# Optimization experiments

Measured on AMD Instinct MI355X. Metric: run time of the kernel, lower is better.

## Reference

```python
import jax, jax.numpy as jnp
import numpy as np

B, N, D, H, F = 2, 2048, 512, 8, 2048
HD = D // H
EPS = 1e-5

def _ln(x, g, b):
    m = jnp.mean(x, axis=-1, keepdims=True)
    v = jnp.mean((x - m) ** 2, axis=-1, keepdims=True)
    return (x - m) * jax.lax.rsqrt(v + EPS) * g + b

def setup_inputs() -> dict:
    key = jax.random.key(0)
    ks = jax.random.split(key, 20)
    def lin(k, din, dout, std=0.05):
        kw, kb = jax.random.split(k)
        return (jax.random.normal(kw, (din, dout), jnp.float32) * std,
                jnp.zeros((dout,), jnp.float32))
    Wq, bq = lin(ks[0], D, D)
    Wk, bk = lin(ks[1], D, D)
    Wv, bv = lin(ks[2], D, D)
    Wg, bg = lin(ks[3], D, D)
    Wo, bo = lin(ks[4], D, D)
    W1, b1 = lin(ks[5], D, F)
    W2, b2 = lin(ks[6], F, D)
    return {
        'x': jax.random.normal(ks[7], (B, N, D), jnp.float32),
        'attn_bias': jax.random.normal(ks[8], (B, N, N, H), jnp.float32) * 0.1,
        'attn_mask': jnp.zeros((B, N, N), jnp.bool_),
        'Wq': Wq, 'bq': bq, 'Wk': Wk, 'bk': bk, 'Wv': Wv, 'bv': bv,
        'Wg': Wg, 'bg': bg, 'Wo': Wo, 'bo': bo,
        'ln1_g': jnp.ones((D,), jnp.float32), 'ln1_b': jnp.zeros((D,), jnp.float32),
        'ln2_g': jnp.ones((D,), jnp.float32), 'ln2_b': jnp.zeros((D,), jnp.float32),
        'W1': W1, 'b1': b1, 'W2': W2, 'b2': b2,
    }

def reference(x, attn_bias, attn_mask, Wq, bq, Wk, bk, Wv, bv, Wg, bg, Wo, bo,
              ln1_g, ln1_b, ln2_g, ln2_b, W1, b1, W2, b2):
    scaling = HD ** -0.5
    # --- self-attention sublayer (pre-LN) ---
    y = _ln(x, ln1_g, ln1_b)
    q = (y @ Wq + bq).reshape(B, N, H, HD) * scaling
    k = (y @ Wk + bk).reshape(B, N, H, HD)
    v = (y @ Wv + bv).reshape(B, N, H, HD)
    u = y * jax.nn.sigmoid(y @ Wg + bg)            # GLU gating branch
    scores = jnp.einsum('bqhd,bkhd->bqkh', q, k)   # [B, Nq, Nk, H]
    scores = scores + attn_bias                    # attn_bias_type == 'add'
    scores = jnp.where(attn_mask[..., None], -jnp.inf, scores)
    w = jax.nn.softmax(scores, axis=2)             # softmax over keys
    attn = jnp.einsum('bqkh,bkhd->bqhd', w, v).reshape(B, N, D)
    attn = attn @ Wo + bo
    y = u + attn
    x = x + y                                      # residual (dropout = identity, eval)
    # --- FFN sublayer (pre-LN) ---
    y = _ln(x, ln2_g, ln2_b)
    y = jax.nn.gelu(y @ W1 + b1, approximate=False) @ W2 + b2
    return x + y
```

## Files before the change

### kernel.cpp

```cpp
#include <hip/hip_runtime.h>
#include <hip/hip_bf16.h>

#define DI __device__ __forceinline__

typedef __attribute__((ext_vector_type(8))) __bf16 bf16x8;
typedef __attribute__((ext_vector_type(4))) float f32x4;
typedef __attribute__((ext_vector_type(4))) unsigned short u16x4;
typedef __attribute__((ext_vector_type(8))) unsigned short u16x8;

DI unsigned short f2bs(float f) {
  __hip_bfloat16 h = __float2bfloat16(f);
  return __builtin_bit_cast(unsigned short, h);
}
DI float bs2f(unsigned short s) {
  return __bfloat162float(__builtin_bit_cast(__hip_bfloat16, s));
}
DI f32x4 mfma16(bf16x8 a, bf16x8 b, f32x4 c) {
  return __builtin_amdgcn_mfma_f32_16x16x32_bf16(a, b, c, 0, 0, 0);
}
DI void g2lds16(const void* g, void* l) {
  __builtin_amdgcn_global_load_lds(
      (__attribute__((address_space(1))) void*)(unsigned long long)g,
      (__attribute__((address_space(3))) void*)l, 16, 0, 0);
}
DI void block_sync_lds() {
  asm volatile("s_waitcnt lgkmcnt(0)" ::: "memory");
  __builtin_amdgcn_sched_barrier(0);
  __builtin_amdgcn_s_barrier();
  __builtin_amdgcn_sched_barrier(0);
}

__global__ __launch_bounds__(256) void k_transw(const float* __restrict__ W,
                                                unsigned short* __restrict__ Wt,
                                                int K, int N) {
  __shared__ float tile[64][65];
  int tk = blockIdx.x * 64, tn = blockIdx.y * 64;
  int t = threadIdx.x;
#pragma unroll
  for (int i = 0; i < 16; ++i) {
    int idx = t + i * 256;
    int r = idx >> 6, c = idx & 63;
    tile[r][c] = W[(size_t)(tk + r) * N + tn + c];
  }
  __syncthreads();
#pragma unroll
  for (int i = 0; i < 16; ++i) {
    int idx = t + i * 256;
    int n = idx >> 6, kk = idx & 63;
    Wt[(size_t)(tn + n) * K + tk + kk] = f2bs(tile[kk][n]);
  }
}

__global__ __launch_bounds__(256) void k_bcat(const float* __restrict__ bq,
                                              const float* __restrict__ bk,
                                              const float* __restrict__ bv,
                                              const float* __restrict__ bg,
                                              float* __restrict__ bcat) {
  int t = blockIdx.x * 256 + threadIdx.x;
  const float* src = t < 512 ? bq : t < 1024 ? bk : t < 1536 ? bv : bg;
  bcat[t] = src[t & 511];
}

__global__ __launch_bounds__(256) void k_ln(const float* __restrict__ x,
                                            const float* __restrict__ g,
                                            const float* __restrict__ b,
                                            unsigned short* __restrict__ y) {
  int row = blockIdx.x, t = threadIdx.x;
  const float* xr = x + (size_t)row * 512;
  float a0 = xr[t], a1 = xr[t + 256];
  float s1 = a0 + a1, s2 = a0 * a0 + a1 * a1;
#pragma unroll
  for (int o = 32; o > 0; o >>= 1) {
    s1 += __shfl_down(s1, o);
    s2 += __shfl_down(s2, o);
  }
  __shared__ float r1[4], r2[4], bc[2];
  int w = t >> 6, l = t & 63;
  if (l == 0) { r1[w] = s1; r2[w] = s2; }
  __syncthreads();
  if (t == 0) {
    float t1 = r1[0] + r1[1] + r1[2] + r1[3];
    float t2 = r2[0] + r2[1] + r2[2] + r2[3];
    float m = t1 / 512.f;
    float v = t2 / 512.f - m * m;
    bc[0] = m;
    bc[1] = rsqrtf(v + 1e-5f);
  }
  __syncthreads();
  float m = bc[0], inv = bc[1];
  y[(size_t)row * 512 + t] = f2bs((a0 - m) * inv * g[t] + b[t]);
  y[(size_t)row * 512 + t + 256] = f2bs((a1 - m) * inv * g[t + 256] + b[t + 256]);
}

template <int BM>
__global__ __launch_bounds__(256) void k_gemm(
    const unsigned short* __restrict__ A, const unsigned short* __restrict__ Bt,
    const float* __restrict__ bias, int M, int N, int K, int mode,
    float* __restrict__ outf, unsigned short* __restrict__ outh,
    const float* __restrict__ add1, const float* __restrict__ add2,
    unsigned short* __restrict__ vtout) {
  constexpr int MI = BM / 32;
  __shared__ __align__(16) unsigned short lA[BM * 64];
  __shared__ __align__(16) unsigned short lB[64 * 64];
  int t = threadIdx.x, w = t >> 6, l = t & 63;
  int l15 = l & 15, lg = l >> 4;
  int m0 = blockIdx.x * BM, n0 = blockIdx.y * 64;
  int wm = (w >> 1) * (BM / 2), wn = (w & 1) * 32;
  f32x4 acc[MI][2] = {};
  int sr = l >> 3, scb = (l & 7) * 16;
  for (int k0 = 0; k0 < K; k0 += 64) {
#pragma unroll
    for (int c = 0; c < MI; ++c) {
      int row = w * (BM / 4) + sr + c * 8;
      g2lds16((const char*)A + ((size_t)(m0 + row) * K + k0) * 2 + scb,
              (char*)lA + w * (BM / 4) * 128 + c * 1024);
    }
#pragma unroll
    for (int c = 0; c < 2; ++c) {
      int row = w * 16 + sr + c * 8;
      g2lds16((const char*)Bt + ((size_t)(n0 + row) * K + k0) * 2 + scb,
              (char*)lB + w * 2048 + c * 1024);
    }
    __syncthreads();
#pragma unroll
    for (int kc = 0; kc < 2; ++kc) {
      bf16x8 af[MI], bfr[2];
#pragma unroll
      for (int i = 0; i < MI; ++i)
        af[i] = *(const bf16x8*)((const char*)lA + (wm + i * 16 + l15) * 128 + kc * 64 + lg * 16);
#pragma unroll
      for (int j = 0; j < 2; ++j)
        bfr[j] = *(const bf16x8*)((const char*)lB + (wn + j * 16 + l15) * 128 + kc * 64 + lg * 16);
#pragma unroll
      for (int i = 0; i < MI; ++i)
#pragma unroll
        for (int j = 0; j < 2; ++j)
          acc[i][j] = mfma16(af[i], bfr[j], acc[i][j]);
    }
    __syncthreads();
  }
#pragma unroll
  for (int i = 0; i < MI; ++i) {
#pragma unroll
    for (int j = 0; j < 2; ++j) {
      int col = n0 + wn + j * 16 + l15;
      int row0 = m0 + wm + i * 16 + lg * 4;
      float vals[4];
#pragma unroll
      for (int r = 0; r < 4; ++r) vals[r] = acc[i][j][r] + bias[col];
      if (mode == 6) {
        int sel = col >> 9, c5 = col & 511;
        if (sel == 2) {
          int hh = c5 >> 6, dd = c5 & 63, bb = row0 >> 11, nn = row0 & 2047;
          u16x4 pk;
#pragma unroll
          for (int r = 0; r < 4; ++r) pk[r] = f2bs(vals[r]);
          *(u16x4*)(vtout + (((size_t)(bb * 8 + hh) * 64 + dd) * 2048 + nn)) = pk;
        } else {
#pragma unroll
          for (int r = 0; r < 4; ++r) {
            size_t idx = (size_t)(row0 + r) * 512 + c5;
            if (sel == 0) outh[idx] = f2bs(vals[r] * 0.125f);
            else if (sel == 1) outh[2097152 + idx] = f2bs(vals[r]);
            else outf[idx] = bs2f(A[idx]) * (1.f / (1.f + __expf(-vals[r])));
          }
        }
      } else {
#pragma unroll
        for (int r = 0; r < 4; ++r) {
          size_t idx = (size_t)(row0 + r) * N + col;
          if (mode == 3) outf[idx] = vals[r] + add1[idx] + add2[idx];
          else if (mode == 4) outh[idx] = f2bs(0.5f * vals[r] * (1.f + erff(vals[r] * 0.70710678f)));
          else outf[idx] = vals[r] + add1[idx];
        }
      }
    }
  }
}

template <int NKS>
__global__ __launch_bounds__(512, 4) void k_attn11(
    const unsigned short* __restrict__ q, const unsigned short* __restrict__ kk,
    const unsigned short* __restrict__ vt, const float* __restrict__ bias,
    const unsigned char* __restrict__ mask, unsigned short* __restrict__ opart,
    float* __restrict__ lpart) {
  __shared__ __align__(16) unsigned short lsB[2][16 * 260];
  __shared__ __align__(16) unsigned short ls_p[8][16][36];

  int bid = blockIdx.x;
  int b = bid & 1;
  int rest = bid >> 1;
  int qt = rest & 127;
  int ksp = rest >> 7;
  int q0 = qt * 16;
  int kbase0 = ksp * (2048 / NKS);
  const int ITERS = 2048 / NKS / 32;
  int t = threadIdx.x, w = t >> 6, l = t & 63;
  int l15 = l & 15, lg = l >> 4;
  int h = w;

  bf16x8 qa0 = *(const bf16x8*)(q + ((size_t)(b * 2048 + q0 + l15) * 512 + h * 64 + lg * 8));
  bf16x8 qa1 = *(const bf16x8*)(q + ((size_t)(b * 2048 + q0 + l15) * 512 + h * 64 + 32 + lg * 8));

  union { bf16x8 v; unsigned short s[8]; } uo;
#pragma unroll
  for (int j = 0; j < 8; ++j) uo.s[j] = 0x3F80;
  const bf16x8 vones = uo.v;

  f32x4 oacc[4] = {};
  f32x4 lacc = {};

  const unsigned short* kbase = kk + ((size_t)(b * 2048) + l15) * 512 + h * 64 + lg * 8;
  const unsigned short* vbase = vt + ((size_t)(b * 8 + h) * 64 + l15) * 2048 + lg * 8;

  int qq = t >> 5, kc = t & 31;
  const float* bptr = bias + ((size_t)(b * 2048 + q0 + qq) * 2048 + kc) * 8;
  const unsigned char* mptr = mask + (size_t)(b * 2048 + q0 + qq) * 2048 + kc;
  const unsigned short BN = f2bs(-1e30f);

#define LOADB(BA, BB, MB, kb)                                                \
  do {                                                                       \
    BA = *(const float4*)(bptr + (size_t)(kb) * 8);                          \
    BB = *(const float4*)(bptr + (size_t)(kb) * 8 + 4);                      \
    MB = mptr[kb];                                                           \
  } while (0)
#define WRITEB(buf, BA, BB, MB)                                              \
  do {                                                                       \
    u16x4 o0, o1;                                                            \
    if (MB) {                                                                \
      o0[0] = o0[1] = o0[2] = o0[3] = BN;                                    \
      o1[0] = o1[1] = o1[2] = o1[3] = BN;                                    \
    } else {                                                                 \
      o0[0] = f2bs(BA.x); o0[1] = f2bs(BA.y); o0[2] = f2bs(BA.z);            \
      o0[3] = f2bs(BA.w); o1[0] = f2bs(BB.x); o1[1] = f2bs(BB.y);            \
      o1[2] = f2bs(BB.z); o1[3] = f2bs(BB.w);                                \
    }                                                                        \
    *(u16x4*)&lsB[buf][qq * 260 + kc * 8] = o0;                              \
    *(u16x4*)&lsB[buf][qq * 260 + kc * 8 + 4] = o1;                          \
  } while (0)
#define COMPUTE(buf, kb)                                                     \
  do {                                                                       \
    const unsigned short* kp = kbase + (size_t)(kb)*512;                     \
    bf16x8 k00 = *(const bf16x8*)(kp);                                       \
    bf16x8 k01 = *(const bf16x8*)(kp + 32);                                  \
    bf16x8 k10 = *(const bf16x8*)(kp + 16 * 512);                            \
    bf16x8 k11 = *(const bf16x8*)(kp + 16 * 512 + 32);                       \
    const unsigned short* vp = vbase + (kb);                                 \
    bf16x8 v0 = *(const bf16x8*)(vp);                                        \
    bf16x8 v1 = *(const bf16x8*)(vp + 16 * 2048);                            \
    bf16x8 v2 = *(const bf16x8*)(vp + 32 * 2048);                            \
    bf16x8 v3 = *(const bf16x8*)(vp + 48 * 2048);                            \
    f32x4 sc0 = {}, sc1 = {};                                                \
    sc0 = mfma16(qa0, k00, sc0);                                             \
    sc0 = mfma16(qa1, k01, sc0);                                             \
    sc1 = mfma16(qa0, k10, sc1);                                             \
    sc1 = mfma16(qa1, k11, sc1);                                             \
    _Pragma("unroll") for (int r = 0; r < 4; ++r) {                          \
      int qr = lg * 4 + r;                                                   \
      float b0 = bs2f(lsB[buf][qr * 260 + l15 * 8 + h]);                     \
      float b1 = bs2f(lsB[buf][qr * 260 + (l15 + 16) * 8 + h]);              \
      float p0 = __expf(sc0[r] + b0 - 8.0f);                                 \
      float p1 = __expf(sc1[r] + b1 - 8.0f);                                 \
      ls_p[w][qr][l15] = f2bs(p0);                                           \
      ls_p[w][qr][16 + l15] = f2bs(p1);                                      \
    }                                                                        \
    bf16x8 pa = *(const bf16x8*)&ls_p[w][l15][lg * 8];                       \
    oacc[0] = mfma16(pa, v0, oacc[0]);                                       \
    oacc[1] = mfma16(pa, v1, oacc[1]);                                       \
    oacc[2] = mfma16(pa, v2, oacc[2]);                                       \
    oacc[3] = mfma16(pa, v3, oacc[3]);                                       \
    lacc = mfma16(pa, vones, lacc);                                          \
  } while (0)

  float4 bA0, bA1, bB0, bB1;
  unsigned char mA, mB;
  LOADB(bA0, bA1, mA, kbase0);
  WRITEB(0, bA0, bA1, mA);
  LOADB(bB0, bB1, mB, kbase0 + 32);
  block_sync_lds();
  for (int it = 0; it < ITERS; it += 2) {
    int kb2 = (it + 2 < ITERS) ? kbase0 + (it + 2) * 32 : kbase0;
    LOADB(bA0, bA1, mA, kb2);
    COMPUTE(0, kbase0 + it * 32);
    WRITEB(1, bB0, bB1, mB);
    block_sync_lds();
    int kb3 = (it + 3 < ITERS) ? kbase0 + (it + 3) * 32 : kbase0;
    LOADB(bB0, bB1, mB, kb3);
    COMPUTE(1, kbase0 + (it + 1) * 32);
    WRITEB(0, bA0, bA1, mA);
    block_sync_lds();
  }
#undef LOADB
#undef WRITEB
#undef COMPUTE

#pragma unroll
  for (int d = 0; d < 4; ++d)
#pragma unroll
    for (int r = 0; r < 4; ++r) {
      size_t row = (size_t)(ksp * 4096 + b * 2048 + q0 + lg * 4 + r);
      opart[row * 512 + h * 64 + d * 16 + l15] = f2bs(oacc[d][r]);
    }
  if (l15 == 0) {
#pragma unroll
    for (int r = 0; r < 4; ++r) {
      size_t row = (size_t)(ksp * 4096 + b * 2048 + q0 + lg * 4 + r);
      lpart[row * 8 + h] = lacc[r];
    }
  }
}

template <int NKS>
__global__ __launch_bounds__(256) void k_comb2(const unsigned short* __restrict__ op,
                                               const float* __restrict__ lp,
                                               unsigned short* __restrict__ ao) {
  int row = blockIdx.x, t = threadIdx.x;
  for (int c = t; c < 512; c += 256) {
    int h = c >> 6;
    float L = 0.f, o = 0.f;
#pragma unroll
    for (int s = 0; s < NKS; ++s) {
      L += lp[(size_t)(s * 4096 + row) * 8 + h];
      o += bs2f(op[(size_t)(s * 4096 + row) * 512 + c]);
    }
    ao[(size_t)row * 512 + c] = f2bs(o / L);
  }
}

extern "C" void kernel_launch(void* const* d_in, const int* in_sizes, int n_in,
                              void* d_out, int out_size, void* d_ws, size_t ws_size,
                              hipStream_t stream) {
  (void)in_sizes; (void)n_in; (void)out_size; (void)ws_size;
  const float* x = (const float*)d_in[0];
  const float* abias = (const float*)d_in[1];
  const unsigned char* amask = (const unsigned char*)d_in[2];
  const float* Wq = (const float*)d_in[3];
  const float* bq = (const float*)d_in[4];
  const float* Wk = (const float*)d_in[5];
  const float* bk = (const float*)d_in[6];
  const float* Wv = (const float*)d_in[7];
  const float* bv = (const float*)d_in[8];
  const float* Wg = (const float*)d_in[9];
  const float* bg = (const float*)d_in[10];
  const float* Wo = (const float*)d_in[11];
  const float* bo = (const float*)d_in[12];
  const float* ln1g = (const float*)d_in[13];
  const float* ln1b = (const float*)d_in[14];
  const float* ln2g = (const float*)d_in[15];
  const float* ln2b = (const float*)d_in[16];
  const float* W1 = (const float*)d_in[17];
  const float* b1 = (const float*)d_in[18];
  const float* W2 = (const float*)d_in[19];
  const float* b2 = (const float*)d_in[20];
  float* outp = (float*)d_out;

  char* ws = (char*)d_ws;
  const size_t MB = 1024 * 1024;

  unsigned short* qb = (unsigned short*)(ws + 0);
  unsigned short* kb = (unsigned short*)(ws + 4 * MB);
  unsigned short* ao = (unsigned short*)(ws + 8 * MB);
  unsigned short* opart = (unsigned short*)(ws + 12 * MB);
  unsigned short* y1 = (unsigned short*)(ws + 28 * MB);
  unsigned short* h1 = (unsigned short*)(ws + 0);
  float* u = (float*)(ws + 32 * MB);
  unsigned short* wcat = (unsigned short*)(ws + 40 * MB);
  unsigned short* wot = (unsigned short*)(ws + 42 * MB);
  unsigned short* w1t = (unsigned short*)(ws + 42 * MB + 512 * 1024);
  unsigned short* w2t = (unsigned short*)(ws + 44 * MB + 512 * 1024);
  float* bcat = (float*)(ws + 46 * MB + 512 * 1024);
  float* lpart = (float*)(ws + 47 * MB);
  unsigned short* vtb = (unsigned short*)(ws + 48 * MB);
  float* x2 = (float*)d_out;

  k_transw<<<dim3(8, 8), 256, 0, stream>>>(Wq, wcat + 0 * 512 * 512, 512, 512);
  k_transw<<<dim3(8, 8), 256, 0, stream>>>(Wk, wcat + 1 * 512 * 512, 512, 512);
  k_transw<<<dim3(8, 8), 256, 0, stream>>>(Wv, wcat + 2 * 512 * 512, 512, 512);
  k_transw<<<dim3(8, 8), 256, 0, stream>>>(Wg, wcat + 3 * 512 * 512, 512, 512);
  k_transw<<<dim3(8, 8), 256, 0, stream>>>(Wo, wot, 512, 512);
  k_transw<<<dim3(8, 32), 256, 0, stream>>>(W1, w1t, 512, 2048);
  k_transw<<<dim3(32, 8), 256, 0, stream>>>(W2, w2t, 2048, 512);
  k_bcat<<<8, 256, 0, stream>>>(bq, bk, bv, bg, bcat);

  k_ln<<<4096, 256, 0, stream>>>(x, ln1g, ln1b, y1);
  k_gemm<128><<<dim3(32, 32), 256, 0, stream>>>(y1, wcat, bcat, 4096, 2048, 512, 6,
                                                u, qb, nullptr, nullptr, vtb);
  k_attn11<4><<<1024, 512, 0, stream>>>(qb, kb, vtb, abias, amask, opart, lpart);
  k_comb2<4><<<4096, 256, 0, stream>>>(opart, lpart, ao);
  k_gemm<64><<<dim3(64, 8), 256, 0, stream>>>(ao, wot, bo, 4096, 512, 512, 3,
                                              x2, nullptr, u, x, nullptr);
  k_ln<<<4096, 256, 0, stream>>>(x2, ln2g, ln2b, y1);
  k_gemm<128><<<dim3(32, 32), 256, 0, stream>>>(y1, w1t, b1, 4096, 2048, 512, 4,
                                                nullptr, h1, nullptr, nullptr, nullptr);
  k_gemm<64><<<dim3(64, 8), 256, 0, stream>>>(h1, w2t, b2, 4096, 512, 2048, 5,
                                              outp, nullptr, x2, nullptr, nullptr);
}
```

Before: 297.7 us.

## Pre-transpose attention bias to per-head bf16 layout and restructure attention blocks

```diff
diff --git a/kernel.cpp b/kernel.cpp
--- a/kernel.cpp
+++ b/kernel.cpp
@@ -23,12 +23,7 @@
       (__attribute__((address_space(1))) void*)(unsigned long long)g,
       (__attribute__((address_space(3))) void*)l, 16, 0, 0);
 }
-DI void block_sync_lds() {
-  asm volatile("s_waitcnt lgkmcnt(0)" ::: "memory");
-  __builtin_amdgcn_sched_barrier(0);
-  __builtin_amdgcn_s_barrier();
-  __builtin_amdgcn_sched_barrier(0);
-}
+#define SB __builtin_amdgcn_sched_barrier(0)
 
 __global__ __launch_bounds__(256) void k_transw(const float* __restrict__ W,
                                                 unsigned short* __restrict__ Wt,
@@ -59,6 +54,49 @@
   int t = blockIdx.x * 256 + threadIdx.x;
   const float* src = t < 512 ? bq : t < 1024 ? bk : t < 1536 ? bv : bg;
   bcat[t] = src[t & 511];
+}
+
+__global__ __launch_bounds__(256) void k_btrans2(const float* __restrict__ bias,
+                                                 const unsigned char* __restrict__ mask,
+                                                 unsigned short* __restrict__ biasT) {
+  __shared__ unsigned short lsT[8][2048];
+  __shared__ unsigned char lsM[2048];
+  int bid = blockIdx.x;
+  int b = bid >> 11, row = bid & 2047;
+  int t = threadIdx.x;
+  size_t rowoff = (size_t)bid * 2048;
+  const float4* src4 = (const float4*)(bias + rowoff * 8);
+#pragma unroll
+  for (int i = 0; i < 16; ++i) {
+    int idx = i * 256 + t;
+    float4 f = src4[idx];
+    int flat = idx * 4;
+    int col = flat >> 3;
+    int h0 = flat & 7;
+    lsT[h0 + 0][col] = f2bs(f.x);
+    lsT[h0 + 1][col] = f2bs(f.y);
+    lsT[h0 + 2][col] = f2bs(f.z);
+    lsT[h0 + 3][col] = f2bs(f.w);
+  }
+  ((uint2*)lsM)[t] = ((const uint2*)(mask + rowoff))[t];
+  __syncthreads();
+  int h = t >> 5, j = t & 31;
+  const unsigned short BN = f2bs(-1e30f);
+  unsigned short* dst = biasT + ((size_t)(b * 8 + h) * 2048 + row) * 2048;
+#pragma unroll
+  for (int s = 0; s < 8; ++s) {
+    int ebase = s * 256 + j * 8;
+    int c32 = (ebase >> 5) << 5;
+    int p0 = ebase & 31;
+    u16x8 o;
+#pragma unroll
+    for (int qq = 0; qq < 8; ++qq) {
+      int p = p0 + qq;
+      int c = c32 + (p >> 1) + ((p & 1) << 4);
+      o[qq] = lsM[c] ? BN : lsT[h][c];
+    }
+    *(u16x8*)(dst + ebase) = o;
+  }
 }
 
 __global__ __launch_bounds__(256) void k_ln(const float* __restrict__ x,
@@ -179,25 +217,22 @@
 }
 
 template <int NKS>
-__global__ __launch_bounds__(512, 4) void k_attn11(
+__global__ __launch_bounds__(256, 4) void k_attn13(
     const unsigned short* __restrict__ q, const unsigned short* __restrict__ kk,
-    const unsigned short* __restrict__ vt, const float* __restrict__ bias,
-    const unsigned char* __restrict__ mask, unsigned short* __restrict__ opart,
-    float* __restrict__ lpart) {
-  __shared__ __align__(16) unsigned short lsB[2][16 * 260];
-  __shared__ __align__(16) unsigned short ls_p[8][16][36];
-
+    const unsigned short* __restrict__ vt, const unsigned short* __restrict__ biasT,
+    unsigned short* __restrict__ opart, float* __restrict__ lpart) {
+  __shared__ unsigned short ls_p[2][4][16][36];
   int bid = blockIdx.x;
   int b = bid & 1;
   int rest = bid >> 1;
   int qt = rest & 127;
-  int ksp = rest >> 7;
+  int rest2 = rest >> 7;
+  int hh = rest2 & 1;
+  int ksp = rest2 >> 1;
   int q0 = qt * 16;
-  int kbase0 = ksp * (2048 / NKS);
-  const int ITERS = 2048 / NKS / 32;
   int t = threadIdx.x, w = t >> 6, l = t & 63;
   int l15 = l & 15, lg = l >> 4;
-  int h = w;
+  int h = hh * 4 + w;
 
   bf16x8 qa0 = *(const bf16x8*)(q + ((size_t)(b * 2048 + q0 + l15) * 512 + h * 64 + lg * 8));
   bf16x8 qa1 = *(const bf16x8*)(q + ((size_t)(b * 2048 + q0 + l15) * 512 + h * 64 + 32 + lg * 8));
@@ -210,89 +245,66 @@
   f32x4 oacc[4] = {};
   f32x4 lacc = {};
 
-  const unsigned short* kbase = kk + ((size_t)(b * 2048) + l15) * 512 + h * 64 + lg * 8;
-  const unsigned short* vbase = vt + ((size_t)(b * 8 + h) * 64 + l15) * 2048 + lg * 8;
-
-  int qq = t >> 5, kc = t & 31;
-  const float* bptr = bias + ((size_t)(b * 2048 + q0 + qq) * 2048 + kc) * 8;
-  const unsigned char* mptr = mask + (size_t)(b * 2048 + q0 + qq) * 2048 + kc;
-  const unsigned short BN = f2bs(-1e30f);
-
-#define LOADB(BA, BB, MB, kb)                                                \
-  do {                                                                       \
-    BA = *(const float4*)(bptr + (size_t)(kb) * 8);                          \
-    BB = *(const float4*)(bptr + (size_t)(kb) * 8 + 4);                      \
-    MB = mptr[kb];                                                           \
+  const int kbase0 = ksp * (2048 / NKS);
+  const int ITERS = 2048 / NKS / 32;
+
+  const unsigned short* krow = kk + ((size_t)(b * 2048) + l15) * 512 + h * 64 + lg * 8;
+  const unsigned short* vrow = vt + (((size_t)(b * 8 + h) * 64) + l15) * 2048 + lg * 8;
+  const unsigned short* brow =
+      biasT + ((size_t)((b * 8 + h) * 2048 + q0 + lg * 4)) * 2048 + l15 * 2;
+
+  bf16x8 kA[4], vA[4], kB[4], vB[4];
+  unsigned bwA[4], bwB[4];
+
+#define LOADT(KR, VR, BW, kb)                                              \
+  do {                                                                     \
+    KR[0] = *(const bf16x8*)(krow + (size_t)(kb) * 512);                   \
+    KR[1] = *(const bf16x8*)(krow + (size_t)(kb) * 512 + 32);              \
+    KR[2] = *(const bf16x8*)(krow + (size_t)((kb) + 16) * 512);            \
+    KR[3] = *(const bf16x8*)(krow + (size_t)((kb) + 16) * 512 + 32);       \
+    BW[0] = *(const unsigned*)(brow + (kb));                               \
+    BW[1] = *(const unsigned*)(brow + 2048 + (kb));                        \
+    BW[2] = *(const unsigned*)(brow + 4096 + (kb));                        \
+    BW[3] = *(const unsigned*)(brow + 6144 + (kb));                        \
+    VR[0] = *(const bf16x8*)(vrow + (kb));                                 \
+    VR[1] = *(const bf16x8*)(vrow + 16 * 2048 + (kb));                     \
+    VR[2] = *(const bf16x8*)(vrow + 32 * 2048 + (kb));                     \
+    VR[3] = *(const bf16x8*)(vrow + 48 * 2048 + (kb));                     \
   } while (0)
-#define WRITEB(buf, BA, BB, MB)                                              \
-  do {                                                                       \
-    u16x4 o0, o1;                                                            \
-    if (MB) {                                                                \
-      o0[0] = o0[1] = o0[2] = o0[3] = BN;                                    \
-      o1[0] = o1[1] = o1[2] = o1[3] = BN;                                    \
-    } else {                                                                 \
-      o0[0] = f2bs(BA.x); o0[1] = f2bs(BA.y); o0[2] = f2bs(BA.z);            \
-      o0[3] = f2bs(BA.w); o1[0] = f2bs(BB.x); o1[1] = f2bs(BB.y);            \
-      o1[2] = f2bs(BB.z); o1[3] = f2bs(BB.w);                                \
-    }                                                                        \
-    *(u16x4*)&lsB[buf][qq * 260 + kc * 8] = o0;                              \
-    *(u16x4*)&lsB[buf][qq * 260 + kc * 8 + 4] = o1;                          \
+
+#define STEP(KR, VR, BW, pb)                                               \
+  do {                                                                     \
+    f32x4 sc0 = {}, sc1 = {};                                              \
+    sc0 = mfma16(qa0, KR[0], sc0);                                         \
+    sc0 = mfma16(qa1, KR[1], sc0);                                         \
+    sc1 = mfma16(qa0, KR[2], sc1);                                         \
+    sc1 = mfma16(qa1, KR[3], sc1);                                         \
+    _Pragma("unroll") for (int r = 0; r < 4; ++r) {                        \
+      float p0 = __expf(sc0[r] + bs2f((unsigned short)(BW[r] & 0xffff)) - 8.0f); \
+      float p1 = __expf(sc1[r] + bs2f((unsigned short)(BW[r] >> 16)) - 8.0f);    \
+      ls_p[pb][w][lg * 4 + r][l15] = f2bs(p0);                             \
+      ls_p[pb][w][lg * 4 + r][16 + l15] = f2bs(p1);                        \
+    }                                                                      \
+    bf16x8 pa = *(const bf16x8*)&ls_p[pb][w][l15][lg * 8];                 \
+    oacc[0] = mfma16(pa, VR[0], oacc[0]);                                  \
+    oacc[1] = mfma16(pa, VR[1], oacc[1]);                                  \
+    oacc[2] = mfma16(pa, VR[2], oacc[2]);                                  \
+    oacc[3] = mfma16(pa, VR[3], oacc[3]);                                  \
+    lacc = mfma16(pa, vones, lacc);                                        \
   } while (0)
-#define COMPUTE(buf, kb)                                                     \
-  do {                                                                       \
-    const unsigned short* kp = kbase + (size_t)(kb)*512;                     \
-    bf16x8 k00 = *(const bf16x8*)(kp);                                       \
-    bf16x8 k01 = *(const bf16x8*)(kp + 32);                                  \
-    bf16x8 k10 = *(const bf16x8*)(kp + 16 * 512);                            \
-    bf16x8 k11 = *(const bf16x8*)(kp + 16 * 512 + 32);                       \
-    const unsigned short* vp = vbase + (kb);                                 \
-    bf16x8 v0 = *(const bf16x8*)(vp);                                        \
-    bf16x8 v1 = *(const bf16x8*)(vp + 16 * 2048);                            \
-    bf16x8 v2 = *(const bf16x8*)(vp + 32 * 2048);                            \
-    bf16x8 v3 = *(const bf16x8*)(vp + 48 * 2048);                            \
-    f32x4 sc0 = {}, sc1 = {};                                                \
-    sc0 = mfma16(qa0, k00, sc0);                                             \
-    sc0 = mfma16(qa1, k01, sc0);                                             \
-    sc1 = mfma16(qa0, k10, sc1);                                             \
-    sc1 = mfma16(qa1, k11, sc1);                                             \
-    _Pragma("unroll") for (int r = 0; r < 4; ++r) {                          \
-      int qr = lg * 4 + r;                                                   \
-      float b0 = bs2f(lsB[buf][qr * 260 + l15 * 8 + h]);                     \
-      float b1 = bs2f(lsB[buf][qr * 260 + (l15 + 16) * 8 + h]);              \
-      float p0 = __expf(sc0[r] + b0 - 8.0f);                                 \
-      float p1 = __expf(sc1[r] + b1 - 8.0f);                                 \
-      ls_p[w][qr][l15] = f2bs(p0);                                           \
-      ls_p[w][qr][16 + l15] = f2bs(p1);                                      \
-    }                                                                        \
-    bf16x8 pa = *(const bf16x8*)&ls_p[w][l15][lg * 8];                       \
-    oacc[0] = mfma16(pa, v0, oacc[0]);                                       \
-    oacc[1] = mfma16(pa, v1, oacc[1]);                                       \
-    oacc[2] = mfma16(pa, v2, oacc[2]);                                       \
-    oacc[3] = mfma16(pa, v3, oacc[3]);                                       \
-    lacc = mfma16(pa, vones, lacc);                                          \
-  } while (0)
-
-  float4 bA0, bA1, bB0, bB1;
-  unsigned char mA, mB;
-  LOADB(bA0, bA1, mA, kbase0);
-  WRITEB(0, bA0, bA1, mA);
-  LOADB(bB0, bB1, mB, kbase0 + 32);
-  block_sync_lds();
+
   for (int it = 0; it < ITERS; it += 2) {
-    int kb2 = (it + 2 < ITERS) ? kbase0 + (it + 2) * 32 : kbase0;
-    LOADB(bA0, bA1, mA, kb2);
-    COMPUTE(0, kbase0 + it * 32);
-    WRITEB(1, bB0, bB1, mB);
-    block_sync_lds();
-    int kb3 = (it + 3 < ITERS) ? kbase0 + (it + 3) * 32 : kbase0;
-    LOADB(bB0, bB1, mB, kb3);
-    COMPUTE(1, kbase0 + (it + 1) * 32);
-    WRITEB(0, bA0, bA1, mA);
-    block_sync_lds();
-  }
-#undef LOADB
-#undef WRITEB
-#undef COMPUTE
+    int kbA = kbase0 + it * 32;
+    int kbB = kbase0 + (it + 1) * 32;
+    SB;
+    LOADT(kA, vA, bwA, kbA);
+    LOADT(kB, vB, bwB, kbB);
+    SB;
+    STEP(kA, vA, bwA, 0);
+    STEP(kB, vB, bwB, 1);
+  }
+#undef LOADT
+#undef STEP
 
 #pragma unroll
   for (int d = 0; d < 4; ++d)
@@ -371,6 +383,7 @@
   float* bcat = (float*)(ws + 46 * MB + 512 * 1024);
   float* lpart = (float*)(ws + 47 * MB);
   unsigned short* vtb = (unsigned short*)(ws + 48 * MB);
+  unsigned short* biasT = (unsigned short*)(ws + 64 * MB);
   float* x2 = (float*)d_out;
 
   k_transw<<<dim3(8, 8), 256, 0, stream>>>(Wq, wcat + 0 * 512 * 512, 512, 512);
@@ -382,11 +395,13 @@
   k_transw<<<dim3(32, 8), 256, 0, stream>>>(W2, w2t, 2048, 512);
   k_bcat<<<8, 256, 0, stream>>>(bq, bk, bv, bg, bcat);
 
+  k_btrans2<<<4096, 256, 0, stream>>>(abias, amask, biasT);
+
   k_ln<<<4096, 256, 0, stream>>>(x, ln1g, ln1b, y1);
   k_gemm<128><<<dim3(32, 32), 256, 0, stream>>>(y1, wcat, bcat, 4096, 2048, 512, 6,
                                                 u, qb, nullptr, nullptr, vtb);
-  k_attn11<4><<<1024, 512, 0, stream>>>(qb, kb, vtb, abias, amask, opart, lpart);
-  k_comb2<4><<<4096, 256, 0, stream>>>(opart, lpart, ao);
+  k_attn13<2><<<1024, 256, 0, stream>>>(qb, kb, vtb, biasT, opart, lpart);
+  k_comb2<2><<<4096, 256, 0, stream>>>(opart, lpart, ao);
   k_gemm<64><<<dim3(64, 8), 256, 0, stream>>>(ao, wot, bo, 4096, 512, 512, 3,
                                               x2, nullptr, u, x, nullptr);
   k_ln<<<4096, 256, 0, stream>>>(x2, ln2g, ln2b, y1);
```

Measured after the change: 355.1 us. 1.19x slower.
